# Kernel tuning notes

Hardware: AMD Instinct MI355X
Metric: run time of the kernel (lower is better)

Reference implementation:

```python
import jax, jax.numpy as jnp
from jax import lax
import numpy as np

B, T, H, K = 128, 256, 768, 64


def setup_inputs() -> dict:
    key = jax.random.key(0)
    k1, k2, k3, k4 = jax.random.split(key, 4)
    hidden = jax.random.normal(k1, (B, T, H), dtype=jnp.float32)
    masks = jnp.ones((B, T), dtype=jnp.int32)
    target = jax.random.randint(k2, (B, T), 0, K, dtype=jnp.int32)
    W = jax.random.normal(k3, (H, K), dtype=jnp.float32) * 0.02
    b = jnp.zeros((K,), dtype=jnp.float32)
    transitions = jax.random.uniform(k4, (K, K), dtype=jnp.float32)
    return {"hidden": hidden, "masks": masks, "target": target,
            "W": W, "b": b, "transitions": transitions}


def _crf_log_norm(emissions, trans, seq_len):
    # emissions: [B,T,K]; forward algorithm (log-sum-exp recurrence over time)
    Tn = emissions.shape[1]
    alpha0 = emissions[:, 0]  # [B,K]

    def step(alpha, xs):
        emis_t, t = xs
        new = jax.nn.logsumexp(alpha[:, :, None] + trans[None], axis=1) + emis_t
        alpha = jnp.where((t < seq_len)[:, None], new, alpha)
        return alpha, None

    xs = (jnp.swapaxes(emissions[:, 1:], 0, 1), jnp.arange(1, Tn))
    alpha, _ = lax.scan(step, alpha0, xs)
    return jax.nn.logsumexp(alpha, axis=1)  # [B]


def _crf_sequence_score(emissions, tags, trans, seq_len):
    Tn = emissions.shape[1]
    t_idx = jnp.arange(Tn)
    valid = t_idx[None, :] < seq_len[:, None]  # [B,T]
    unary = jnp.take_along_axis(emissions, tags[..., None], axis=2)[..., 0]
    unary = jnp.sum(jnp.where(valid, unary, 0.0), axis=1)
    pair = trans[tags[:, :-1], tags[:, 1:]]  # [B,T-1]
    valid_pair = t_idx[1:][None, :] < seq_len[:, None]
    binary = jnp.sum(jnp.where(valid_pair, pair, 0.0), axis=1)
    return unary + binary


def _crf_decode(emissions, trans, seq_len):
    # Viterbi with backpointers; padded steps carry state (identity backptr)
    Bn, Tn, Kn = emissions.shape
    v0 = emissions[:, 0]

    def step(v, xs):
        emis_t, t = xs
        scores = v[:, :, None] + trans[None]  # [B, K_prev, K_cur]
        bp = jnp.argmax(scores, axis=1).astype(jnp.int32)
        new_v = jnp.max(scores, axis=1) + emis_t
        m = (t < seq_len)[:, None]
        v = jnp.where(m, new_v, v)
        bp = jnp.where(m, bp, jnp.arange(Kn, dtype=jnp.int32)[None])
        return v, bp

    xs = (jnp.swapaxes(emissions[:, 1:], 0, 1), jnp.arange(1, Tn))
    v, bps = lax.scan(step, v0, xs)  # bps: [T-1, B, K]
    best_score = jnp.max(v, axis=1)
    last_tag = jnp.argmax(v, axis=1).astype(jnp.int32)

    def back(tag, bp_t):
        prev = jnp.take_along_axis(bp_t, tag[:, None], axis=1)[:, 0]
        return prev, prev

    _, rev_tags = lax.scan(back, last_tag, bps, reverse=True)  # [T-1, B]
    path = jnp.concatenate([rev_tags, last_tag[None]], axis=0)  # [T, B]
    path = jnp.swapaxes(path, 0, 1)  # [B, T]
    valid = jnp.arange(Tn)[None, :] < seq_len[:, None]
    path = jnp.where(valid, path, 0)
    return path, best_score


def reference(hidden, masks, target, W, b, transitions):
    # dense projection (dropout omitted for determinism)
    emissions = jnp.einsum('bth,hk->btk', hidden, W) + b  # [B,T,K]
    seq_len = jnp.sum(masks, axis=1).astype(jnp.int32)
    log_norm = _crf_log_norm(emissions, transitions, seq_len)
    seq_score = _crf_sequence_score(emissions, target, transitions, seq_len)
    log_likelihood = seq_score - log_norm  # [B]
    decode_predict, _crf_scores = _crf_decode(emissions, transitions, seq_len)
    return decode_predict, log_likelihood
```

## Files before the change

kernel.cpp:

```cpp
#include <hip/hip_runtime.h>

#define B_ 128
#define T_ 256
#define H_ 768
#define K_ 64
#define BT_ (B_ * T_)

__global__ __launch_bounds__(256) void gemm_emis(const float* __restrict__ hidden,
                                                 const float* __restrict__ W,
                                                 const float* __restrict__ bias,
                                                 float* __restrict__ emis) {
    __shared__ float At[128 * 65];
    __shared__ float Wt[64 * 64];

    const int tid = threadIdx.x;
    const int tx = tid & 15;
    const int ty = tid >> 4;
    const int rowbase = blockIdx.x * 128;

    float acc[8][4];
#pragma unroll
    for (int r = 0; r < 8; ++r)
#pragma unroll
        for (int c = 0; c < 4; ++c) acc[r][c] = 0.f;

    for (int hb = 0; hb < H_; hb += 64) {
#pragma unroll
        for (int k = 0; k < 8; ++k) {
            int f = tid + k * 256;
            int row = f >> 4;
            int hq = f & 15;
            float4 v = *(const float4*)&hidden[(size_t)(rowbase + row) * H_ + hb + hq * 4];
            At[row * 65 + hq * 4 + 0] = v.x;
            At[row * 65 + hq * 4 + 1] = v.y;
            At[row * 65 + hq * 4 + 2] = v.z;
            At[row * 65 + hq * 4 + 3] = v.w;
        }
#pragma unroll
        for (int k = 0; k < 4; ++k) {
            int f = tid + k * 256;
            int wr = f >> 4;
            int wc = f & 15;
            float4 v = *(const float4*)&W[(size_t)(hb + wr) * K_ + wc * 4];
            *(float4*)&Wt[wr * 64 + wc * 4] = v;
        }
        __syncthreads();
#pragma unroll 8
        for (int h = 0; h < 64; ++h) {
            float4 wv = *(float4*)&Wt[h * 64 + tx * 4];
#pragma unroll
            for (int r = 0; r < 8; ++r) {
                float av = At[(ty * 8 + r) * 65 + h];
                acc[r][0] += av * wv.x;
                acc[r][1] += av * wv.y;
                acc[r][2] += av * wv.z;
                acc[r][3] += av * wv.w;
            }
        }
        __syncthreads();
    }

    float4 bv = *(const float4*)&bias[tx * 4];
#pragma unroll
    for (int r = 0; r < 8; ++r) {
        float4 o;
        o.x = acc[r][0] + bv.x;
        o.y = acc[r][1] + bv.y;
        o.z = acc[r][2] + bv.z;
        o.w = acc[r][3] + bv.w;
        *(float4*)&emis[(size_t)(rowbase + ty * 8 + r) * K_ + tx * 4] = o;
    }
}

__global__ __launch_bounds__(64) void crf_kernel(const float* __restrict__ emis,
                                                 const int* __restrict__ masks,
                                                 const int* __restrict__ target,
                                                 const float* __restrict__ trans,
                                                 float* __restrict__ out) {
    __shared__ unsigned char bpb[255 * 64];
    __shared__ float fbuf[64];
    __shared__ int pathb[256];

    const int lane = threadIdx.x;
    const int bid = blockIdx.x;
    const int b = (bid < B_) ? bid : bid - B_;

    int sl = 0;
#pragma unroll
    for (int k = 0; k < 4; ++k) sl += masks[b * T_ + lane + k * 64];
#pragma unroll
    for (int m = 32; m; m >>= 1) sl += __shfl_xor(sl, m, 64);
    const int seq_len = sl;

    const float* eb = emis + (size_t)b * (T_ * K_);

    if (bid < B_) {
        float Ecol[64];
#pragma unroll
        for (int i = 0; i < 64; ++i) Ecol[i] = __expf(trans[i * K_ + lane]);

        float a = eb[lane];
        float e_t = eb[K_ + lane];
        for (int t = 1; t < T_; ++t) {
            float e_next = (t < T_ - 1) ? eb[(t + 1) * K_ + lane] : 0.f;
            float m0 = __shfl(a, 0, 64);
            float p = __expf(a - m0);
            fbuf[lane] = p;
            float s0 = 0.f, s1 = 0.f, s2 = 0.f, s3 = 0.f;
#pragma unroll
            for (int i = 0; i < 16; ++i) {
                float4 p4 = *(float4*)&fbuf[i * 4];
                s0 += p4.x * Ecol[i * 4 + 0];
                s1 += p4.y * Ecol[i * 4 + 1];
                s2 += p4.z * Ecol[i * 4 + 2];
                s3 += p4.w * Ecol[i * 4 + 3];
            }
            float na = m0 + __logf((s0 + s1) + (s2 + s3)) + e_t;
            if (t < seq_len) a = na;
            e_t = e_next;
        }
        float mm = a;
#pragma unroll
        for (int m = 32; m; m >>= 1) mm = fmaxf(mm, __shfl_xor(mm, m, 64));
        float ex = __expf(a - mm);
#pragma unroll
        for (int m = 32; m; m >>= 1) ex += __shfl_xor(ex, m, 64);
        float log_norm = mm + __logf(ex);

        float sc = 0.f;
#pragma unroll
        for (int k = 0; k < 4; ++k) {
            int t = lane + k * 64;
            if (t < seq_len) {
                int tg = target[b * T_ + t];
                sc += eb[t * K_ + tg];
                if (t >= 1) {
                    int tp = target[b * T_ + t - 1];
                    sc += trans[tp * K_ + tg];
                }
            }
        }
#pragma unroll
        for (int m = 32; m; m >>= 1) sc += __shfl_xor(sc, m, 64);
        if (lane == 0) out[BT_ + b] = sc - log_norm;
    } else {
        float Tcol[64];
#pragma unroll
        for (int i = 0; i < 64; ++i) Tcol[i] = trans[i * K_ + lane];

        float v = eb[lane];
        float e_t = eb[K_ + lane];
        for (int t = 1; t < T_; ++t) {
            float e_next = (t < T_ - 1) ? eb[(t + 1) * K_ + lane] : 0.f;
            fbuf[lane] = v;
            float best = -3.4e38f;
            int bi = 0;
#pragma unroll
            for (int i = 0; i < 16; ++i) {
                float4 v4 = *(float4*)&fbuf[i * 4];
                float s;
                s = v4.x + Tcol[i * 4 + 0]; if (s > best) { best = s; bi = i * 4 + 0; }
                s = v4.y + Tcol[i * 4 + 1]; if (s > best) { best = s; bi = i * 4 + 1; }
                s = v4.z + Tcol[i * 4 + 2]; if (s > best) { best = s; bi = i * 4 + 2; }
                s = v4.w + Tcol[i * 4 + 3]; if (s > best) { best = s; bi = i * 4 + 3; }
            }
            int bp;
            if (t < seq_len) { v = best + e_t; bp = bi; }
            else             { bp = lane; }
            bpb[(t - 1) * 64 + lane] = (unsigned char)bp;
            e_t = e_next;
        }
        float bv = v;
        int bidx = lane;
#pragma unroll
        for (int m = 32; m; m >>= 1) {
            float ov = __shfl_xor(bv, m, 64);
            int oi = __shfl_xor(bidx, m, 64);
            if (ov > bv || (ov == bv && oi < bidx)) { bv = ov; bidx = oi; }
        }
        int tag = bidx;

        pathb[255] = tag;
        for (int t = T_ - 1; t >= 1; --t) {
            tag = bpb[(t - 1) * 64 + tag];
            pathb[t - 1] = tag;
        }
#pragma unroll
        for (int k = 0; k < 4; ++k) {
            int t = lane + k * 64;
            out[b * T_ + t] = (t < seq_len) ? (float)pathb[t] : 0.f;
        }
    }
}

extern "C" void kernel_launch(void* const* d_in, const int* in_sizes, int n_in,
                              void* d_out, int out_size, void* d_ws, size_t ws_size,
                              hipStream_t stream) {
    const float* hidden = (const float*)d_in[0];
    const int* masks    = (const int*)d_in[1];
    const int* target   = (const int*)d_in[2];
    const float* W      = (const float*)d_in[3];
    const float* bias   = (const float*)d_in[4];
    const float* trans  = (const float*)d_in[5];
    float* out = (float*)d_out;
    float* emis = (float*)d_ws;

    gemm_emis<<<dim3(BT_ / 128), dim3(256), 0, stream>>>(hidden, W, bias, emis);
    crf_kernel<<<dim3(2 * B_), dim3(64), 0, stream>>>(emis, masks, target, trans, out);
}
```

Before: 383.8 us.

## Restructure emission GEMM and CRF recurrences with scaled forward and backtrack-by-recompute

The emission GEMM now uses 64-row blocks with W held in registers per lane and float4 LDS reads of the hidden tile. The forward algorithm switches to a scaled-probability recurrence that avoids a per-step exp and shuffle. Viterbi drops per-step argmax tracking: it stores all Viterbi scores in LDS and recovers backpointers during backtracking through DPP wave max reductions and ballots. This shortens the serial per-step chain but adds a wave reduction to each backtrack step, raises LDS use to 80KB per CRF block, and may change tie-breaking and numerical stability.

```diff
diff --git a/kernel.cpp b/kernel.cpp
--- a/kernel.cpp
+++ b/kernel.cpp
@@ -6,80 +6,89 @@
 #define K_ 64
 #define BT_ (B_ * T_)
 
-__global__ __launch_bounds__(256) void gemm_emis(const float* __restrict__ hidden,
-                                                 const float* __restrict__ W,
-                                                 const float* __restrict__ bias,
-                                                 float* __restrict__ emis) {
-    __shared__ float At[128 * 65];
-    __shared__ float Wt[64 * 64];
+template <int CTRL>
+__device__ __forceinline__ float dpp_mov_f(float x) {
+    return __int_as_float(__builtin_amdgcn_update_dpp(
+        __float_as_int(x), __float_as_int(x), CTRL, 0xF, 0xF, false));
+}
+__device__ __forceinline__ float wave_max64(float x) {
+    x = fmaxf(x, dpp_mov_f<0x111>(x));
+    x = fmaxf(x, dpp_mov_f<0x112>(x));
+    x = fmaxf(x, dpp_mov_f<0x114>(x));
+    x = fmaxf(x, dpp_mov_f<0x118>(x));
+    x = fmaxf(x, dpp_mov_f<0x142>(x));
+    x = fmaxf(x, dpp_mov_f<0x143>(x));
+    return __int_as_float(__builtin_amdgcn_readlane(__float_as_int(x), 63));
+}
+__device__ __forceinline__ float readlane0_f(float x) {
+    return __int_as_float(__builtin_amdgcn_readfirstlane(__float_as_int(x)));
+}
+
+__global__ __launch_bounds__(256, 2) void gemm_emis(const float* __restrict__ hidden,
+                                                    const float* __restrict__ W,
+                                                    const float* __restrict__ bias,
+                                                    float* __restrict__ emis) {
+    __shared__ __align__(16) float At[64 * 64];
 
     const int tid = threadIdx.x;
-    const int tx = tid & 15;
-    const int ty = tid >> 4;
-    const int rowbase = blockIdx.x * 128;
-
-    float acc[8][4];
-#pragma unroll
-    for (int r = 0; r < 8; ++r)
-#pragma unroll
-        for (int c = 0; c < 4; ++c) acc[r][c] = 0.f;
+    const int lane = tid & 63;
+    const int wv = tid >> 6;
+    const int rowbase = blockIdx.x * 64;
+    const int r0 = wv * 16;
+
+    float acc[16];
+    const float bb = bias[lane];
+#pragma unroll
+    for (int r = 0; r < 16; ++r) acc[r] = bb;
 
     for (int hb = 0; hb < H_; hb += 64) {
 #pragma unroll
-        for (int k = 0; k < 8; ++k) {
-            int f = tid + k * 256;
-            int row = f >> 4;
-            int hq = f & 15;
-            float4 v = *(const float4*)&hidden[(size_t)(rowbase + row) * H_ + hb + hq * 4];
-            At[row * 65 + hq * 4 + 0] = v.x;
-            At[row * 65 + hq * 4 + 1] = v.y;
-            At[row * 65 + hq * 4 + 2] = v.z;
-            At[row * 65 + hq * 4 + 3] = v.w;
-        }
-#pragma unroll
         for (int k = 0; k < 4; ++k) {
-            int f = tid + k * 256;
-            int wr = f >> 4;
-            int wc = f & 15;
-            float4 v = *(const float4*)&W[(size_t)(hb + wr) * K_ + wc * 4];
-            *(float4*)&Wt[wr * 64 + wc * 4] = v;
-        }
+            int flat = tid + k * 256;
+            int row = flat >> 4;
+            int h4 = flat & 15;
+            *(float4*)&At[row * 64 + h4 * 4] =
+                *(const float4*)&hidden[(size_t)(rowbase + row) * H_ + hb + h4 * 4];
+        }
+        float Wr[64];
+#pragma unroll
+        for (int h = 0; h < 64; ++h) Wr[h] = W[(size_t)(hb + h) * K_ + lane];
         __syncthreads();
-#pragma unroll 8
-        for (int h = 0; h < 64; ++h) {
-            float4 wv = *(float4*)&Wt[h * 64 + tx * 4];
-#pragma unroll
-            for (int r = 0; r < 8; ++r) {
-                float av = At[(ty * 8 + r) * 65 + h];
-                acc[r][0] += av * wv.x;
-                acc[r][1] += av * wv.y;
-                acc[r][2] += av * wv.z;
-                acc[r][3] += av * wv.w;
+
+#pragma unroll
+        for (int rg = 0; rg < 4; ++rg) {
+#pragma unroll
+            for (int h4 = 0; h4 < 16; ++h4) {
+                float4 a0 = *(const float4*)&At[(r0 + rg * 4 + 0) * 64 + h4 * 4];
+                float4 a1 = *(const float4*)&At[(r0 + rg * 4 + 1) * 64 + h4 * 4];
+                float4 a2 = *(const float4*)&At[(r0 + rg * 4 + 2) * 64 + h4 * 4];
+                float4 a3 = *(const float4*)&At[(r0 + rg * 4 + 3) * 64 + h4 * 4];
+                float w0 = Wr[h4 * 4 + 0], w1 = Wr[h4 * 4 + 1];
+                float w2 = Wr[h4 * 4 + 2], w3 = Wr[h4 * 4 + 3];
+                acc[rg * 4 + 0] += a0.x * w0; acc[rg * 4 + 0] += a0.y * w1;
+                acc[rg * 4 + 0] += a0.z * w2; acc[rg * 4 + 0] += a0.w * w3;
+                acc[rg * 4 + 1] += a1.x * w0; acc[rg * 4 + 1] += a1.y * w1;
+                acc[rg * 4 + 1] += a1.z * w2; acc[rg * 4 + 1] += a1.w * w3;
+                acc[rg * 4 + 2] += a2.x * w0; acc[rg * 4 + 2] += a2.y * w1;
+                acc[rg * 4 + 2] += a2.z * w2; acc[rg * 4 + 2] += a2.w * w3;
+                acc[rg * 4 + 3] += a3.x * w0; acc[rg * 4 + 3] += a3.y * w1;
+                acc[rg * 4 + 3] += a3.z * w2; acc[rg * 4 + 3] += a3.w * w3;
             }
         }
         __syncthreads();
     }
-
-    float4 bv = *(const float4*)&bias[tx * 4];
-#pragma unroll
-    for (int r = 0; r < 8; ++r) {
-        float4 o;
-        o.x = acc[r][0] + bv.x;
-        o.y = acc[r][1] + bv.y;
-        o.z = acc[r][2] + bv.z;
-        o.w = acc[r][3] + bv.w;
-        *(float4*)&emis[(size_t)(rowbase + ty * 8 + r) * K_ + tx * 4] = o;
-    }
-}
-
-__global__ __launch_bounds__(64) void crf_kernel(const float* __restrict__ emis,
-                                                 const int* __restrict__ masks,
-                                                 const int* __restrict__ target,
-                                                 const float* __restrict__ trans,
-                                                 float* __restrict__ out) {
-    __shared__ unsigned char bpb[255 * 64];
-    __shared__ float fbuf[64];
-    __shared__ int pathb[256];
+#pragma unroll
+    for (int r = 0; r < 16; ++r)
+        emis[(size_t)(rowbase + r0 + r) * K_ + lane] = acc[r];
+}
+
+__global__ __launch_bounds__(64, 1) void crf_kernel(const float* __restrict__ emis,
+                                                    const int* __restrict__ masks,
+                                                    const int* __restrict__ target,
+                                                    const float* __restrict__ trans,
+                                                    float* __restrict__ out) {
+    __shared__ __align__(16) float vbuf[T_ * K_];
+    __shared__ float tbuf[K_ * 65];
 
     const int lane = threadIdx.x;
     const int bid = blockIdx.x;
@@ -99,33 +108,41 @@
 #pragma unroll
         for (int i = 0; i < 64; ++i) Ecol[i] = __expf(trans[i * K_ + lane]);
 
-        float a = eb[lane];
-        float e_t = eb[K_ + lane];
+        float e0 = eb[lane];
+        float a00 = readlane0_f(e0);
+        float r = __expf(e0 - a00);
+        float c = a00;
+
+        float e_cur = eb[K_ + lane];
+        float e0_cur = readlane0_f(e_cur);
+        float x_cur = __expf(e_cur - e0_cur);
+
         for (int t = 1; t < T_; ++t) {
-            float e_next = (t < T_ - 1) ? eb[(t + 1) * K_ + lane] : 0.f;
-            float m0 = __shfl(a, 0, 64);
-            float p = __expf(a - m0);
-            fbuf[lane] = p;
+            float e_nxt = (t < T_ - 1) ? eb[(t + 1) * K_ + lane] : 0.f;
+            vbuf[lane] = r;
             float s0 = 0.f, s1 = 0.f, s2 = 0.f, s3 = 0.f;
 #pragma unroll
             for (int i = 0; i < 16; ++i) {
-                float4 p4 = *(float4*)&fbuf[i * 4];
+                float4 p4 = *(const float4*)&vbuf[i * 4];
                 s0 += p4.x * Ecol[i * 4 + 0];
                 s1 += p4.y * Ecol[i * 4 + 1];
                 s2 += p4.z * Ecol[i * 4 + 2];
                 s3 += p4.w * Ecol[i * 4 + 3];
             }
-            float na = m0 + __logf((s0 + s1) + (s2 + s3)) + e_t;
-            if (t < seq_len) a = na;
-            e_t = e_next;
-        }
-        float mm = a;
-#pragma unroll
-        for (int m = 32; m; m >>= 1) mm = fmaxf(mm, __shfl_xor(mm, m, 64));
-        float ex = __expf(a - mm);
-#pragma unroll
-        for (int m = 32; m; m >>= 1) ex += __shfl_xor(ex, m, 64);
-        float log_norm = mm + __logf(ex);
+            float S = (s0 + s1) + (s2 + s3);
+            float S0 = readlane0_f(S);
+            if (t < seq_len) {
+                r = __fdividef(S * x_cur, S0);
+                c += __logf(S0) + e0_cur;
+            }
+            e_cur = e_nxt;
+            e0_cur = readlane0_f(e_cur);
+            x_cur = __expf(e_cur - e0_cur);
+        }
+        float rs = r;
+#pragma unroll
+        for (int m = 32; m; m >>= 1) rs += __shfl_xor(rs, m, 64);
+        float log_norm = c + __logf(rs);
 
         float sc = 0.f;
 #pragma unroll
@@ -134,10 +151,7 @@
             if (t < seq_len) {
                 int tg = target[b * T_ + t];
                 sc += eb[t * K_ + tg];
-                if (t >= 1) {
-                    int tp = target[b * T_ + t - 1];
-                    sc += trans[tp * K_ + tg];
-                }
+                if (t >= 1) sc += trans[target[b * T_ + t - 1] * K_ + tg];
             }
         }
 #pragma unroll
@@ -147,48 +161,56 @@
         float Tcol[64];
 #pragma unroll
         for (int i = 0; i < 64; ++i) Tcol[i] = trans[i * K_ + lane];
+        for (int idx = lane; idx < K_ * K_; idx += 64)
+            tbuf[(idx >> 6) * 65 + (idx & 63)] = trans[idx];
 
         float v = eb[lane];
-        float e_t = eb[K_ + lane];
+        vbuf[lane] = v;
+        float e_cur = eb[K_ + lane];
         for (int t = 1; t < T_; ++t) {
-            float e_next = (t < T_ - 1) ? eb[(t + 1) * K_ + lane] : 0.f;
-            fbuf[lane] = v;
-            float best = -3.4e38f;
-            int bi = 0;
+            float e_nxt = (t < T_ - 1) ? eb[(t + 1) * K_ + lane] : 0.f;
+            const float* vp = &vbuf[(t - 1) * K_];
+            float mm[4];
+            mm[0] = mm[1] = mm[2] = mm[3] = -3.4e38f;
 #pragma unroll
             for (int i = 0; i < 16; ++i) {
-                float4 v4 = *(float4*)&fbuf[i * 4];
-                float s;
-                s = v4.x + Tcol[i * 4 + 0]; if (s > best) { best = s; bi = i * 4 + 0; }
-                s = v4.y + Tcol[i * 4 + 1]; if (s > best) { best = s; bi = i * 4 + 1; }
-                s = v4.z + Tcol[i * 4 + 2]; if (s > best) { best = s; bi = i * 4 + 2; }
-                s = v4.w + Tcol[i * 4 + 3]; if (s > best) { best = s; bi = i * 4 + 3; }
-            }
-            int bp;
-            if (t < seq_len) { v = best + e_t; bp = bi; }
-            else             { bp = lane; }
-            bpb[(t - 1) * 64 + lane] = (unsigned char)bp;
-            e_t = e_next;
-        }
-        float bv = v;
-        int bidx = lane;
-#pragma unroll
-        for (int m = 32; m; m >>= 1) {
-            float ov = __shfl_xor(bv, m, 64);
-            int oi = __shfl_xor(bidx, m, 64);
-            if (ov > bv || (ov == bv && oi < bidx)) { bv = ov; bidx = oi; }
-        }
-        int tag = bidx;
-
-        pathb[255] = tag;
+                float4 v4 = *(const float4*)&vp[i * 4];
+                float q = fmaxf(fmaxf(v4.x + Tcol[i * 4 + 0], v4.y + Tcol[i * 4 + 1]),
+                                fmaxf(v4.z + Tcol[i * 4 + 2], v4.w + Tcol[i * 4 + 3]));
+                mm[i & 3] = fmaxf(mm[i & 3], q);
+            }
+            float M = fmaxf(fmaxf(mm[0], mm[1]), fmaxf(mm[2], mm[3]));
+            if (t < seq_len) v = M + e_cur;
+            vbuf[t * K_ + lane] = v;
+            e_cur = e_nxt;
+        }
+
+        float M = wave_max64(v);
+        unsigned long long ball = __ballot(v >= M);
+        int tag = (int)__builtin_ctzll(ball);
+
+        int path[4];
+#pragma unroll
+        for (int k = 0; k < 4; ++k) path[k] = 0;
+        if (lane == ((T_ - 1) & 63)) path[(T_ - 1) >> 6] = tag;
+
+        float vpre = vbuf[(T_ - 2) * K_ + lane];
         for (int t = T_ - 1; t >= 1; --t) {
-            tag = bpb[(t - 1) * 64 + tag];
-            pathb[t - 1] = tag;
+            float vnext = (t >= 2) ? vbuf[(t - 2) * K_ + lane] : 0.f;
+            if (t < seq_len) {
+                float s = vpre + tbuf[lane * 65 + tag];
+                float Ms = wave_max64(s);
+                unsigned long long bl = __ballot(s >= Ms);
+                tag = (int)__builtin_ctzll(bl);
+            }
+            int p = t - 1;
+            if (lane == (p & 63)) path[p >> 6] = tag;
+            vpre = vnext;
         }
 #pragma unroll
         for (int k = 0; k < 4; ++k) {
             int t = lane + k * 64;
-            out[b * T_ + t] = (t < seq_len) ? (float)pathb[t] : 0.f;
+            out[b * T_ + t] = (t < seq_len) ? (float)path[k] : 0.f;
         }
     }
 }
@@ -205,6 +227,6 @@
     float* out = (float*)d_out;
     float* emis = (float*)d_ws;
 
-    gemm_emis<<<dim3(BT_ / 128), dim3(256), 0, stream>>>(hidden, W, bias, emis);
+    gemm_emis<<<dim3(BT_ / 64), dim3(256), 0, stream>>>(hidden, W, bias, emis);
     crf_kernel<<<dim3(2 * B_), dim3(64), 0, stream>>>(emis, masks, target, trans, out);
 }
```

Result: slower. 414.4 us (+8.0%).
